# Kernel optimization log

Hardware: AMD Instinct MI355X
Metric: run time of the kernel (lower is better)

Reference implementation:

```python
import jax, jax.numpy as jnp
import numpy as np

SIZE = (160, 192, 160)  # matches init_kwargs `size`


def _make_grid(size):
    # torch: meshgrid(arange(s) for s, indexing='ij'), stack last dim, flip last dim
    vecs = [jnp.arange(s, dtype=jnp.float32) for s in size]
    g = jnp.stack(jnp.meshgrid(*vecs, indexing='ij'), axis=-1)
    g = g[..., ::-1]  # last-dim order becomes (x, y, z) = (W, H, D) indices
    return g[None]    # [1, D, H, W, 3]


def _grid_sample_3d(src, locs):
    """Trilinear grid_sample, align_corners=True, padding_mode='zeros'.
    src: [B, C, D, H, W]; locs: [B, D, H, W, 3] in [-1,1], last dim (x,y,z)."""
    B, C, D, H, W = src.shape
    dims_m1 = jnp.array([W - 1, H - 1, D - 1], jnp.float32)
    px = (locs + 1.0) * 0.5 * dims_m1  # unnormalize (align_corners=True)
    x, y, z = px[..., 0], px[..., 1], px[..., 2]
    x0 = jnp.floor(x); y0 = jnp.floor(y); z0 = jnp.floor(z)
    fx, fy, fz = x - x0, y - y0, z - z0
    x0i = x0.astype(jnp.int32); y0i = y0.astype(jnp.int32); z0i = z0.astype(jnp.int32)

    def gather(src_b, iz, iy, ix):  # src_b: [C,D,H,W]; idx: [D,H,W]
        return src_b[:, iz, iy, ix]  # [C,D,H,W]

    out = jnp.zeros(src.shape, src.dtype)
    for dz in (0, 1):
        for dy in (0, 1):
            for dx in (0, 1):
                ix, iy, iz = x0i + dx, y0i + dy, z0i + dz
                valid = (ix >= 0) & (ix < W) & (iy >= 0) & (iy < H) & (iz >= 0) & (iz < D)
                w = ((fx if dx else 1.0 - fx)
                     * (fy if dy else 1.0 - fy)
                     * (fz if dz else 1.0 - fz))
                w = jnp.where(valid, w, 0.0)  # zero padding for OOB
                icx = jnp.clip(ix, 0, W - 1)
                icy = jnp.clip(iy, 0, H - 1)
                icz = jnp.clip(iz, 0, D - 1)
                v = jax.vmap(gather)(src, icz, icy, icx)  # [B,C,D,H,W]
                out = out + w[:, None] * v
    return out


def setup_inputs() -> dict:
    key = jax.random.key(0)
    k1, k2 = jax.random.split(key)
    B, C = 2, 2
    D, H, W = SIZE
    src = jax.random.normal(k1, (B, C, D, H, W), dtype=jnp.float32)
    flow = jax.random.normal(k2, (B, 3, D, H, W), dtype=jnp.float32)
    return {"src": src, "flow": flow}


def reference(src, flow):
    # order='image': no flip of flow channels
    flow = jnp.moveaxis(flow, 1, -1)                      # [B,D,H,W,3]
    grid = _make_grid(SIZE)                                # [1,D,H,W,3]
    s = jnp.array(SIZE, jnp.float32)[::-1] - 1.0           # [W-1,H-1,D-1]
    new_locs = 2.0 * ((grid + flow) / s - 0.5)             # normalized [-1,1]
    return _grid_sample_3d(src, new_locs)
```

## Files before the change

kernel.cpp:

```cpp
#include <hip/hip_runtime.h>

#define DD 160
#define HH 192
#define WW 160
#define SP (DD * HH * WW)
#define NB 2
#define NC 2

#define TX 32
#define TY 8
#define TZ 4
#define RXW 40
#define RYH 15
#define RZD 11
#define REGC (RZD * RYH * RXW)
#define NCHUNK (REGC / 4)
#define NITER 7

#define NTX 5
#define NTY 24
#define NTZ 40
#define NTILES (NTX * NTY * NTZ * NB)
#define PER_XCD (NTILES / 8)

typedef float v2f __attribute__((ext_vector_type(2)));
typedef float v4f __attribute__((ext_vector_type(4)));

__device__ __forceinline__ v4f ld4_nt(const float* p) {
    return __builtin_nontemporal_load(reinterpret_cast<const v4f*>(p));
}
__device__ __forceinline__ void st4_nt(float* p, v4f v) {
    __builtin_nontemporal_store(v, reinterpret_cast<v4f*>(p));
}
__device__ __forceinline__ v2f ld2g(const float* p) {
    return *reinterpret_cast<const v2f*>(p);
}
__device__ __forceinline__ v2f s2(float f) { v2f v = {f, f}; return v; }

__device__ __forceinline__ void sample_global(
    const float* __restrict__ s0, const float* __restrict__ s1,
    int x, int y, int z, float dx, float dy, float dz,
    float& a0, float& a1)
{
    float sx = (float)x + dx, sy = (float)y + dy, sz = (float)z + dz;
    float xf = floorf(sx), yf = floorf(sy), zf = floorf(sz);
    float fx = sx - xf, fy = sy - yf, fz = sz - zf;
    int x0 = (int)xf, y0 = (int)yf, z0 = (int)zf;
    int x1 = x0 + 1, y1 = y0 + 1, z1 = z0 + 1;

    float wx0 = (x0 >= 0 && x0 < WW) ? (1.0f - fx) : 0.0f;
    float wx1 = (x1 >= 0 && x1 < WW) ? fx : 0.0f;
    float wy0 = (y0 >= 0 && y0 < HH) ? (1.0f - fy) : 0.0f;
    float wy1 = (y1 >= 0 && y1 < HH) ? fy : 0.0f;
    float wz0 = (z0 >= 0 && z0 < DD) ? (1.0f - fz) : 0.0f;
    float wz1 = (z1 >= 0 && z1 < DD) ? fz : 0.0f;

    int p  = min(max(x0, 0), WW - 2);
    int i0 = min(max(x0, 0), WW - 1) - p;
    int i1 = min(max(x1, 0), WW - 1) - p;
    int cy0 = min(max(y0, 0), HH - 1), cy1 = min(max(y1, 0), HH - 1);
    int cz0 = min(max(z0, 0), DD - 1), cz1 = min(max(z1, 0), DD - 1);

    int o00 = (cz0 * HH + cy0) * WW + p;
    int o01 = (cz0 * HH + cy1) * WW + p;
    int o10 = (cz1 * HH + cy0) * WW + p;
    int o11 = (cz1 * HH + cy1) * WW + p;

    float w00 = wz0 * wy0, w01 = wz0 * wy1, w10 = wz1 * wy0, w11 = wz1 * wy1;

    v2f c0_00 = ld2g(s0 + o00); v2f c1_00 = ld2g(s1 + o00);
    v2f c0_01 = ld2g(s0 + o01); v2f c1_01 = ld2g(s1 + o01);
    v2f c0_10 = ld2g(s0 + o10); v2f c1_10 = ld2g(s1 + o10);
    v2f c0_11 = ld2g(s0 + o11); v2f c1_11 = ld2g(s1 + o11);

    #define PICK(v, i) ((i) ? (v).y : (v).x)
    float r0, r1;
    r0  = w00 * (wx0 * PICK(c0_00, i0) + wx1 * PICK(c0_00, i1));
    r1  = w00 * (wx0 * PICK(c1_00, i0) + wx1 * PICK(c1_00, i1));
    r0 += w01 * (wx0 * PICK(c0_01, i0) + wx1 * PICK(c0_01, i1));
    r1 += w01 * (wx0 * PICK(c1_01, i0) + wx1 * PICK(c1_01, i1));
    r0 += w10 * (wx0 * PICK(c0_10, i0) + wx1 * PICK(c0_10, i1));
    r1 += w10 * (wx0 * PICK(c1_10, i0) + wx1 * PICK(c1_10, i1));
    r0 += w11 * (wx0 * PICK(c0_11, i0) + wx1 * PICK(c0_11, i1));
    r1 += w11 * (wx0 * PICK(c1_11, i0) + wx1 * PICK(c1_11, i1));
    #undef PICK
    a0 = r0; a1 = r1;
}

__global__ __launch_bounds__(256, 3) void st_warp_kernel(
    const float* __restrict__ src,
    const float* __restrict__ flow,
    float* __restrict__ out)
{
    __shared__ float sbuf[2 * REGC];

    int u   = blockIdx.x;
    int tl  = (u & 7) * PER_XCD + (u >> 3);
    int tx  = tl % NTX;  int t2 = tl / NTX;
    int ty  = t2 % NTY;  int t3 = t2 / NTY;
    int tz  = t3 % NTZ;  int b  = t3 / NTZ;
    int X0 = tx * TX, Y0 = ty * TY, Z0 = tz * TZ;
    int tid = threadIdx.x;

    const float* sb = src + b * NC * SP;

    v4f va[NITER], vb[NITER];
    int  ad[NITER];
    #pragma unroll
    for (int i = 0; i < NITER; ++i) {
        int c = tid + i * 256;
        if (i < NITER - 1 || c < NCHUNK) {
            int lz  = c / 150;  int r2 = c - lz * 150;
            int ly  = r2 / 10;  int lxc = r2 - ly * 10;
            int mz = min(max(Z0 - 3 + lz, 0), DD - 1);
            int my = min(max(Y0 - 3 + ly, 0), HH - 1);
            int mx = X0 - 4 + lxc * 4;
            const float* p = sb + (mz * HH + my) * WW;
            v4f A, B;
            if (mx >= 0 && mx <= WW - 4) {
                A = *reinterpret_cast<const v4f*>(p + mx);
                B = *reinterpret_cast<const v4f*>(p + SP + mx);
            } else {
                int m0 = min(max(mx,     0), WW - 1);
                int m1 = min(max(mx + 1, 0), WW - 1);
                int m2 = min(max(mx + 2, 0), WW - 1);
                int m3 = min(max(mx + 3, 0), WW - 1);
                A.x = p[m0]; A.y = p[m1]; A.z = p[m2]; A.w = p[m3];
                B.x = p[SP + m0]; B.y = p[SP + m1]; B.z = p[SP + m2]; B.w = p[SP + m3];
            }
            va[i] = A; vb[i] = B;
            ad[i] = 2 * ((lz * RYH + ly) * RXW + lxc * 4);
        } else {
            ad[i] = -1;
        }
    }

    int rr = tid >> 3;
    int xi = (tid & 7) << 2;
    int yl = rr & 7, zl = rr >> 3;
    int y = Y0 + yl, z = Z0 + zl, x = X0 + xi;
    int fo = b * 3 * SP + (z * HH + y) * WW + x;
    v4f dxv = ld4_nt(flow + fo);
    v4f dyv = ld4_nt(flow + fo + SP);
    v4f dzv = ld4_nt(flow + fo + 2 * SP);

    #pragma unroll
    for (int i = 0; i < NITER; ++i) {
        if (ad[i] >= 0) {
            v4f w0 = {va[i].x, vb[i].x, va[i].y, vb[i].y};
            v4f w1 = {va[i].z, vb[i].z, va[i].w, vb[i].w};
            *reinterpret_cast<v4f*>(&sbuf[ad[i]])     = w0;
            *reinterpret_cast<v4f*>(&sbuf[ad[i] + 4]) = w1;
        }
    }
    __syncthreads();

    const int rx0 = X0 - 4, ry0 = Y0 - 3, rz0 = Z0 - 3;
    float a0[4], a1[4];
    #pragma unroll
    for (int j = 0; j < 4; ++j) {
        float dx = dxv[j], dy = dyv[j], dz = dzv[j];
        bool inH = (dx >= -4.0f) & (dx < 4.0f) &
                   (dy >= -3.0f) & (dy < 4.0f) &
                   (dz >= -3.0f) & (dz < 4.0f);
        if (inH) {
            float lx = (float)(xi + j + 4) + dx;
            float ly = (float)(yl + 3) + dy;
            float lz = (float)(zl + 3) + dz;
            float xf = floorf(lx), yf = floorf(ly), zf = floorf(lz);
            float fx = lx - xf, fy = ly - yf, fz = lz - zf;
            int ix = (int)xf, iy = (int)yf, iz = (int)zf;

            int vx0 = ix + rx0, vy0 = iy + ry0, vz0 = iz + rz0;
            float wx0 = (vx0 >= 0  && vx0 < WW)     ? (1.0f - fx) : 0.0f;
            float wx1 = (vx0 >= -1 && vx0 < WW - 1) ? fx          : 0.0f;
            float wy0 = (vy0 >= 0  && vy0 < HH)     ? (1.0f - fy) : 0.0f;
            float wy1 = (vy0 >= -1 && vy0 < HH - 1) ? fy          : 0.0f;
            float wz0 = (vz0 >= 0  && vz0 < DD)     ? (1.0f - fz) : 0.0f;
            float wz1 = (vz0 >= -1 && vz0 < DD - 1) ? fz          : 0.0f;

            const float* pB = sbuf + 2 * ((iz * RYH + iy) * RXW + ix);
            v2f A00 = *(const v2f*)(pB);
            v2f B00 = *(const v2f*)(pB + 2);
            v2f A01 = *(const v2f*)(pB + 2 * RXW);
            v2f B01 = *(const v2f*)(pB + 2 * RXW + 2);
            const float* pC = pB + 2 * RYH * RXW;
            v2f A10 = *(const v2f*)(pC);
            v2f B10 = *(const v2f*)(pC + 2);
            v2f A11 = *(const v2f*)(pC + 2 * RXW);
            v2f B11 = *(const v2f*)(pC + 2 * RXW + 2);

            v2f c00 = s2(wx0) * A00 + s2(wx1) * B00;
            v2f c01 = s2(wx0) * A01 + s2(wx1) * B01;
            v2f c10 = s2(wx0) * A10 + s2(wx1) * B10;
            v2f c11 = s2(wx0) * A11 + s2(wx1) * B11;
            v2f m0  = s2(wy0) * c00 + s2(wy1) * c01;
            v2f m1  = s2(wy0) * c10 + s2(wy1) * c11;
            v2f r   = s2(wz0) * m0  + s2(wz1) * m1;
            a0[j] = r.x; a1[j] = r.y;
        } else {
            sample_global(sb, sb + SP, x + j, y, z, dx, dy, dz, a0[j], a1[j]);
        }
    }

    int oo = b * NC * SP + (z * HH + y) * WW + x;
    v4f o0 = {a0[0], a0[1], a0[2], a0[3]};
    v4f o1 = {a1[0], a1[1], a1[2], a1[3]};
    st4_nt(out + oo, o0);
    st4_nt(out + oo + SP, o1);
}

extern "C" void kernel_launch(void* const* d_in, const int* in_sizes, int n_in,
                              void* d_out, int out_size, void* d_ws, size_t ws_size,
                              hipStream_t stream) {
    const float* src  = (const float*)d_in[0];
    const float* flow = (const float*)d_in[1];
    float* out = (float*)d_out;

    st_warp_kernel<<<NTILES, 256, 0, stream>>>(src, flow, out);
}
```

Measured before the change: 276.5 us.

## Drop LDS halo staging; gather directly from global with bounds-specialized tiles

Removes the shared-memory halo region load, its transpose and the block-wide barrier. Each output point now gathers its eight corners straight from global memory and relies on L1/L2 for reuse. Interior tiles get template specializations that skip clamping and validity masks, and launch bounds are raised to allow more resident blocks. This gives up the guaranteed on-chip reuse of the staged region in exchange for fewer instructions and no synchronisation, and it risks more cache traffic from scattered 8-byte loads.

```diff
diff --git a/kernel.cpp b/kernel.cpp
--- a/kernel.cpp
+++ b/kernel.cpp
@@ -10,13 +10,6 @@
 #define TX 32
 #define TY 8
 #define TZ 4
-#define RXW 40
-#define RYH 15
-#define RZD 11
-#define REGC (RZD * RYH * RXW)
-#define NCHUNK (REGC / 4)
-#define NITER 7
-
 #define NTX 5
 #define NTY 24
 #define NTZ 40
@@ -35,12 +28,11 @@
 __device__ __forceinline__ v2f ld2g(const float* p) {
     return *reinterpret_cast<const v2f*>(p);
 }
-__device__ __forceinline__ v2f s2(float f) { v2f v = {f, f}; return v; }
+__device__ __forceinline__ float pick(v2f v, int i) { return i ? v.y : v.x; }
 
-__device__ __forceinline__ void sample_global(
-    const float* __restrict__ s0, const float* __restrict__ s1,
-    int x, int y, int z, float dx, float dy, float dz,
-    float& a0, float& a1)
+__device__ __forceinline__ float sample_global1(
+    const float* __restrict__ s,
+    int x, int y, int z, float dx, float dy, float dz)
 {
     float sx = (float)x + dx, sy = (float)y + dy, sz = (float)z + dz;
     float xf = floorf(sx), yf = floorf(sy), zf = floorf(sz);
@@ -66,34 +58,102 @@
     int o10 = (cz1 * HH + cy0) * WW + p;
     int o11 = (cz1 * HH + cy1) * WW + p;
 
-    float w00 = wz0 * wy0, w01 = wz0 * wy1, w10 = wz1 * wy0, w11 = wz1 * wy1;
+    v2f c00 = ld2g(s + o00);
+    v2f c01 = ld2g(s + o01);
+    v2f c10 = ld2g(s + o10);
+    v2f c11 = ld2g(s + o11);
 
-    v2f c0_00 = ld2g(s0 + o00); v2f c1_00 = ld2g(s1 + o00);
-    v2f c0_01 = ld2g(s0 + o01); v2f c1_01 = ld2g(s1 + o01);
-    v2f c0_10 = ld2g(s0 + o10); v2f c1_10 = ld2g(s1 + o10);
-    v2f c0_11 = ld2g(s0 + o11); v2f c1_11 = ld2g(s1 + o11);
-
-    #define PICK(v, i) ((i) ? (v).y : (v).x)
-    float r0, r1;
-    r0  = w00 * (wx0 * PICK(c0_00, i0) + wx1 * PICK(c0_00, i1));
-    r1  = w00 * (wx0 * PICK(c1_00, i0) + wx1 * PICK(c1_00, i1));
-    r0 += w01 * (wx0 * PICK(c0_01, i0) + wx1 * PICK(c0_01, i1));
-    r1 += w01 * (wx0 * PICK(c1_01, i0) + wx1 * PICK(c1_01, i1));
-    r0 += w10 * (wx0 * PICK(c0_10, i0) + wx1 * PICK(c0_10, i1));
-    r1 += w10 * (wx0 * PICK(c1_10, i0) + wx1 * PICK(c1_10, i1));
-    r0 += w11 * (wx0 * PICK(c0_11, i0) + wx1 * PICK(c0_11, i1));
-    r1 += w11 * (wx0 * PICK(c1_11, i0) + wx1 * PICK(c1_11, i1));
-    #undef PICK
-    a0 = r0; a1 = r1;
+    float r;
+    r  = (wz0 * wy0) * (wx0 * pick(c00, i0) + wx1 * pick(c00, i1));
+    r += (wz0 * wy1) * (wx0 * pick(c01, i0) + wx1 * pick(c01, i1));
+    r += (wz1 * wy0) * (wx0 * pick(c10, i0) + wx1 * pick(c10, i1));
+    r += (wz1 * wy1) * (wx0 * pick(c11, i0) + wx1 * pick(c11, i1));
+    return r;
 }
 
-__global__ __launch_bounds__(256, 3) void st_warp_kernel(
+template<bool IX, bool IYZ>
+__device__ __forceinline__ void sample_fast(
+    const float* __restrict__ s0, float sx, float sy, float sz,
+    float& r0, float& r1)
+{
+    float xf = floorf(sx), yf = floorf(sy), zf = floorf(sz);
+    float fx = sx - xf, fy = sy - yf, fz = sz - zf;
+    int ix = (int)xf, iy = (int)yf, iz = (int)zf;
+
+    float wx0, wx1; int px, i0, i1;
+    if (IX) {
+        px = ix; i0 = 0; i1 = 1; wx0 = 1.0f - fx; wx1 = fx;
+    } else {
+        wx0 = (ix >= 0  && ix < WW)     ? (1.0f - fx) : 0.0f;
+        wx1 = (ix >= -1 && ix < WW - 1) ? fx          : 0.0f;
+        px = min(max(ix, 0), WW - 2);
+        i0 = min(max(ix, 0), WW - 1) - px;
+        i1 = min(max(ix + 1, 0), WW - 1) - px;
+    }
+    float wy0, wy1, wz0, wz1; int py0, py1, pz0, pz1;
+    if (IYZ) {
+        py0 = iy; py1 = iy + 1; wy0 = 1.0f - fy; wy1 = fy;
+        pz0 = iz; pz1 = iz + 1; wz0 = 1.0f - fz; wz1 = fz;
+    } else {
+        wy0 = (iy >= 0  && iy < HH)     ? (1.0f - fy) : 0.0f;
+        wy1 = (iy >= -1 && iy < HH - 1) ? fy          : 0.0f;
+        py0 = min(max(iy, 0), HH - 1);
+        py1 = min(max(iy + 1, 0), HH - 1);
+        wz0 = (iz >= 0  && iz < DD)     ? (1.0f - fz) : 0.0f;
+        wz1 = (iz >= -1 && iz < DD - 1) ? fz          : 0.0f;
+        pz0 = min(max(iz, 0), DD - 1);
+        pz1 = min(max(iz + 1, 0), DD - 1);
+    }
+
+    int o00 = (pz0 * HH + py0) * WW + px;
+    int o01 = (pz0 * HH + py1) * WW + px;
+    int o10 = (pz1 * HH + py0) * WW + px;
+    int o11 = (pz1 * HH + py1) * WW + px;
+
+    v2f A00 = ld2g(s0 + o00), A01 = ld2g(s0 + o01);
+    v2f A10 = ld2g(s0 + o10), A11 = ld2g(s0 + o11);
+    v2f B00 = ld2g(s0 + SP + o00), B01 = ld2g(s0 + SP + o01);
+    v2f B10 = ld2g(s0 + SP + o10), B11 = ld2g(s0 + SP + o11);
+
+    float w00 = wz0 * wy0, w01 = wz0 * wy1, w10 = wz1 * wy0, w11 = wz1 * wy1;
+    #define XL(v) (wx0 * pick(v, i0) + wx1 * pick(v, i1))
+    r0 = w00 * XL(A00) + w01 * XL(A01) + w10 * XL(A10) + w11 * XL(A11);
+    r1 = w00 * XL(B00) + w01 * XL(B01) + w10 * XL(B10) + w11 * XL(B11);
+    #undef XL
+}
+
+template<bool IX, bool IYZ>
+__device__ __forceinline__ void compute_tile(
+    const float* __restrict__ sb, int x, int y, int z,
+    v4f dxv, v4f dyv, v4f dzv, float* __restrict__ op)
+{
+    float a0[4], a1[4];
+    #pragma unroll
+    for (int j = 0; j < 4; ++j) {
+        float dx = dxv[j], dy = dyv[j], dz = dzv[j];
+        bool ok = true;
+        if (IX)  ok = (dx >= -4.0f) & (dx < 4.0f);
+        if (IYZ) ok = ok & (dy >= -4.0f) & (dy < 4.0f) &
+                          (dz >= -4.0f) & (dz < 4.0f);
+        if (ok) {
+            sample_fast<IX, IYZ>(sb, (float)(x + j) + dx, (float)y + dy,
+                                 (float)z + dz, a0[j], a1[j]);
+        } else {
+            a0[j] = sample_global1(sb,      x + j, y, z, dx, dy, dz);
+            a1[j] = sample_global1(sb + SP, x + j, y, z, dx, dy, dz);
+        }
+    }
+    v4f o0 = {a0[0], a0[1], a0[2], a0[3]};
+    v4f o1 = {a1[0], a1[1], a1[2], a1[3]};
+    st4_nt(op, o0);
+    st4_nt(op + SP, o1);
+}
+
+__global__ __launch_bounds__(256, 6) void st_warp_kernel(
     const float* __restrict__ src,
     const float* __restrict__ flow,
     float* __restrict__ out)
 {
-    __shared__ float sbuf[2 * REGC];
-
     int u   = blockIdx.x;
     int tl  = (u & 7) * PER_XCD + (u >> 3);
     int tx  = tl % NTX;  int t2 = tl / NTX;
@@ -102,112 +162,27 @@
     int X0 = tx * TX, Y0 = ty * TY, Z0 = tz * TZ;
     int tid = threadIdx.x;
 
+    int xi = (tid & 7) << 2;
+    int rr = tid >> 3;
+    int yl = rr & 7, zl = rr >> 3;
+    int x = X0 + xi, y = Y0 + yl, z = Z0 + zl;
+
+    int go = (z * HH + y) * WW + x;
     const float* sb = src + b * NC * SP;
+    const float* fp = flow + b * 3 * SP + go;
+    float* op = out + b * NC * SP + go;
 
-    v4f va[NITER], vb[NITER];
-    int  ad[NITER];
-    #pragma unroll
-    for (int i = 0; i < NITER; ++i) {
-        int c = tid + i * 256;
-        if (i < NITER - 1 || c < NCHUNK) {
-            int lz  = c / 150;  int r2 = c - lz * 150;
-            int ly  = r2 / 10;  int lxc = r2 - ly * 10;
-            int mz = min(max(Z0 - 3 + lz, 0), DD - 1);
-            int my = min(max(Y0 - 3 + ly, 0), HH - 1);
-            int mx = X0 - 4 + lxc * 4;
-            const float* p = sb + (mz * HH + my) * WW;
-            v4f A, B;
-            if (mx >= 0 && mx <= WW - 4) {
-                A = *reinterpret_cast<const v4f*>(p + mx);
-                B = *reinterpret_cast<const v4f*>(p + SP + mx);
-            } else {
-                int m0 = min(max(mx,     0), WW - 1);
-                int m1 = min(max(mx + 1, 0), WW - 1);
-                int m2 = min(max(mx + 2, 0), WW - 1);
-                int m3 = min(max(mx + 3, 0), WW - 1);
-                A.x = p[m0]; A.y = p[m1]; A.z = p[m2]; A.w = p[m3];
-                B.x = p[SP + m0]; B.y = p[SP + m1]; B.z = p[SP + m2]; B.w = p[SP + m3];
-            }
-            va[i] = A; vb[i] = B;
-            ad[i] = 2 * ((lz * RYH + ly) * RXW + lxc * 4);
-        } else {
-            ad[i] = -1;
-        }
-    }
+    v4f dxv = ld4_nt(fp);
+    v4f dyv = ld4_nt(fp + SP);
+    v4f dzv = ld4_nt(fp + 2 * SP);
 
-    int rr = tid >> 3;
-    int xi = (tid & 7) << 2;
-    int yl = rr & 7, zl = rr >> 3;
-    int y = Y0 + yl, z = Z0 + zl, x = X0 + xi;
-    int fo = b * 3 * SP + (z * HH + y) * WW + x;
-    v4f dxv = ld4_nt(flow + fo);
-    v4f dyv = ld4_nt(flow + fo + SP);
-    v4f dzv = ld4_nt(flow + fo + 2 * SP);
+    bool xin  = (tx >= 1) & (tx <= 3);
+    bool yzin = (ty >= 1) & (ty <= 22) & (tz >= 1) & (tz <= 38);
 
-    #pragma unroll
-    for (int i = 0; i < NITER; ++i) {
-        if (ad[i] >= 0) {
-            v4f w0 = {va[i].x, vb[i].x, va[i].y, vb[i].y};
-            v4f w1 = {va[i].z, vb[i].z, va[i].w, vb[i].w};
-            *reinterpret_cast<v4f*>(&sbuf[ad[i]])     = w0;
-            *reinterpret_cast<v4f*>(&sbuf[ad[i] + 4]) = w1;
-        }
-    }
-    __syncthreads();
-
-    const int rx0 = X0 - 4, ry0 = Y0 - 3, rz0 = Z0 - 3;
-    float a0[4], a1[4];
-    #pragma unroll
-    for (int j = 0; j < 4; ++j) {
-        float dx = dxv[j], dy = dyv[j], dz = dzv[j];
-        bool inH = (dx >= -4.0f) & (dx < 4.0f) &
-                   (dy >= -3.0f) & (dy < 4.0f) &
-                   (dz >= -3.0f) & (dz < 4.0f);
-        if (inH) {
-            float lx = (float)(xi + j + 4) + dx;
-            float ly = (float)(yl + 3) + dy;
-            float lz = (float)(zl + 3) + dz;
-            float xf = floorf(lx), yf = floorf(ly), zf = floorf(lz);
-            float fx = lx - xf, fy = ly - yf, fz = lz - zf;
-            int ix = (int)xf, iy = (int)yf, iz = (int)zf;
-
-            int vx0 = ix + rx0, vy0 = iy + ry0, vz0 = iz + rz0;
-            float wx0 = (vx0 >= 0  && vx0 < WW)     ? (1.0f - fx) : 0.0f;
-            float wx1 = (vx0 >= -1 && vx0 < WW - 1) ? fx          : 0.0f;
-            float wy0 = (vy0 >= 0  && vy0 < HH)     ? (1.0f - fy) : 0.0f;
-            float wy1 = (vy0 >= -1 && vy0 < HH - 1) ? fy          : 0.0f;
-            float wz0 = (vz0 >= 0  && vz0 < DD)     ? (1.0f - fz) : 0.0f;
-            float wz1 = (vz0 >= -1 && vz0 < DD - 1) ? fz          : 0.0f;
-
-            const float* pB = sbuf + 2 * ((iz * RYH + iy) * RXW + ix);
-            v2f A00 = *(const v2f*)(pB);
-            v2f B00 = *(const v2f*)(pB + 2);
-            v2f A01 = *(const v2f*)(pB + 2 * RXW);
-            v2f B01 = *(const v2f*)(pB + 2 * RXW + 2);
-            const float* pC = pB + 2 * RYH * RXW;
-            v2f A10 = *(const v2f*)(pC);
-            v2f B10 = *(const v2f*)(pC + 2);
-            v2f A11 = *(const v2f*)(pC + 2 * RXW);
-            v2f B11 = *(const v2f*)(pC + 2 * RXW + 2);
-
-            v2f c00 = s2(wx0) * A00 + s2(wx1) * B00;
-            v2f c01 = s2(wx0) * A01 + s2(wx1) * B01;
-            v2f c10 = s2(wx0) * A10 + s2(wx1) * B10;
-            v2f c11 = s2(wx0) * A11 + s2(wx1) * B11;
-            v2f m0  = s2(wy0) * c00 + s2(wy1) * c01;
-            v2f m1  = s2(wy0) * c10 + s2(wy1) * c11;
-            v2f r   = s2(wz0) * m0  + s2(wz1) * m1;
-            a0[j] = r.x; a1[j] = r.y;
-        } else {
-            sample_global(sb, sb + SP, x + j, y, z, dx, dy, dz, a0[j], a1[j]);
-        }
-    }
-
-    int oo = b * NC * SP + (z * HH + y) * WW + x;
-    v4f o0 = {a0[0], a0[1], a0[2], a0[3]};
-    v4f o1 = {a1[0], a1[1], a1[2], a1[3]};
-    st4_nt(out + oo, o0);
-    st4_nt(out + oo + SP, o1);
+    if (xin & yzin)      compute_tile<true,  true >(sb, x, y, z, dxv, dyv, dzv, op);
+    else if (xin)        compute_tile<true,  false>(sb, x, y, z, dxv, dyv, dzv, op);
+    else if (yzin)       compute_tile<false, true >(sb, x, y, z, dxv, dyv, dzv, op);
+    else                 compute_tile<false, false>(sb, x, y, z, dxv, dyv, dzv, op);
 }
 
 extern "C" void kernel_launch(void* const* d_in, const int* in_sizes, int n_in,
```

Result: slower. 387.5 us (+40.2%).
